# Performance work log

Hardware: AMD Instinct MI355X
Metric: run time of the kernel (lower is better)

## Reference

```python
import jax, jax.numpy as jnp
import numpy as np

GDEP = 3
ALPHA = 0.05


def setup_inputs() -> dict:
    key = jax.random.key(0)
    k1, k2, k3, k4 = jax.random.split(key, 4)
    x = jax.random.normal(k1, (8, 32, 512, 512), dtype=jnp.float32)
    adj = jax.random.uniform(k2, (512, 512), dtype=jnp.float32)
    W = jax.random.normal(k3, (32, 128), dtype=jnp.float32) * 0.02  # 1x1 conv weight [c_out, (gdep+1)*c_in]
    b = jax.random.normal(k4, (32,), dtype=jnp.float32) * 0.02
    return {"x": x, "adj": adj, "W": W, "b": b}


def reference(x, adj, W, b):
    # x: [n, c, v, l]; adj: [v, v]
    n_nodes = adj.shape[0]
    a = adj + jnp.eye(n_nodes, dtype=adj.dtype)
    a = a / a.sum(axis=1, keepdims=True)  # row-normalized adjacency
    h = x
    out = [h]
    for _ in range(GDEP):
        h = jnp.einsum('ncwl,vw->ncvl', h, a)       # diffuse over nodes
        h = ALPHA * x + (1.0 - ALPHA) * h           # alpha residual mix
        out.append(h)
    ho = jnp.concatenate(out, axis=1)               # [n, (gdep+1)*c, v, l]
    y = jnp.einsum('ncvl,oc->novl', ho, W) + b[None, :, None, None]  # 1x1 conv
    return y
```

## Files before the change

kernel.cpp:

```cpp
#include <hip/hip_runtime.h>
#include <cstdint>
#include <cstddef>

typedef unsigned short u16;
typedef unsigned int   u32;
typedef __attribute__((ext_vector_type(8))) short bf16x8;
typedef __attribute__((ext_vector_type(4))) float f32x4;

#define ALPHA 0.05f
#define OMA   0.95f

__device__ __forceinline__ u16 f2b(float f) {
  u32 u = __float_as_uint(f);
  u = (u + 0x7fffu + ((u >> 16) & 1u)) >> 16;
  return (u16)u;
}

__device__ __forceinline__ void gld16(const void* g, void* l) {
  __builtin_amdgcn_global_load_lds((const __attribute__((address_space(1))) u32*)g,
                                   (__attribute__((address_space(3))) u32*)l, 16, 0, 0);
}

__global__ __launch_bounds__(256) void k_norm(const float* __restrict__ adj,
                                              float* __restrict__ Af) {
  int v = blockIdx.x;
  int t = threadIdx.x;
  float a0 = adj[(size_t)v * 512 + t]       + (t == v ? 1.f : 0.f);
  float a1 = adj[(size_t)v * 512 + t + 256] + (t + 256 == v ? 1.f : 0.f);
  float s = a0 + a1;
  for (int off = 32; off; off >>= 1) s += __shfl_down(s, off);
  __shared__ float ws4[4];
  if ((t & 63) == 0) ws4[t >> 6] = s;
  __syncthreads();
  float inv = OMA / (ws4[0] + ws4[1] + ws4[2] + ws4[3]);
  Af[(size_t)v * 512 + t]       = a0 * inv;
  Af[(size_t)v * 512 + t + 256] = a1 * inv;
}

__global__ __launch_bounds__(256) void k_pow(const float* __restrict__ L,
                                             const float* __restrict__ R,
                                             float* __restrict__ Pf) {
  __shared__ float lrow[4][512];
  int r0 = blockIdx.x * 4;
  int t = threadIdx.x;
  for (int i = t; i < 4 * 512; i += 256)
    lrow[i >> 9][i & 511] = L[(size_t)(r0 + (i >> 9)) * 512 + (i & 511)];
  __syncthreads();
  float acc[4][2] = {};
  for (int k = 0; k < 512; ++k) {
    float rk0 = R[(size_t)k * 512 + t];
    float rk1 = R[(size_t)k * 512 + t + 256];
#pragma unroll
    for (int r = 0; r < 4; ++r) {
      float lv = lrow[r][k];
      acc[r][0] += lv * rk0;
      acc[r][1] += lv * rk1;
    }
  }
  for (int r = 0; r < 4; ++r) {
    Pf[(size_t)(r0 + r) * 512 + t]       = acc[r][0];
    Pf[(size_t)(r0 + r) * 512 + t + 256] = acc[r][1];
  }
}

__global__ __launch_bounds__(256) void k_pack(const float* __restrict__ A1,
                                              const float* __restrict__ A2,
                                              const float* __restrict__ A3,
                                              u16* __restrict__ G) {
  int v = blockIdx.x;
  int t = threadIdx.x;
#pragma unroll
  for (int h = 0; h < 2; ++h) {
    int w = t + h * 256;
    size_t i = (size_t)v * 512 + w;
    u32 lo = (u32)(w == v ? 0x3F80u : 0u) | ((u32)f2b(A1[i]) << 16);
    u32 hi = (u32)f2b(A2[i]) | ((u32)f2b(A3[i]) << 16);
    *(uint2*)(G + (size_t)v * 2048 + w * 4) = make_uint2(lo, hi);
  }
}

__global__ void k_u(const float* __restrict__ W, u16* __restrict__ U) {
  int R = threadIdx.x;
  int o = R >> 2, j = R & 3;
  for (int c = 0; c < 32; ++c) {
    float w0 = W[o * 128 + c];
    float w1 = W[o * 128 + 32 + c];
    float w2 = W[o * 128 + 64 + c];
    float w3 = W[o * 128 + 96 + c];
    float u;
    if (j == 0)      u = w0 + ALPHA * (w1 + w2 + w3);
    else if (j == 1) u = w1 + ALPHA * (w2 + w3);
    else if (j == 2) u = w2 + ALPHA * w3;
    else             u = w3;
    U[R * 32 + c] = f2b(u);
  }
}

__global__ __launch_bounds__(256) void k_mix(const float* __restrict__ x,
                                             const u16* __restrict__ Uw,
                                             u16* __restrict__ C,
                                             int n0) {
  __shared__ u16 slab[512 * 32];
  __shared__ u16 Ul[128 * 32];
  int t = threadIdx.x;
  int chunk = gridDim.x >> 3;
  int rb = blockIdx.x;
  int virt = (rb & 7) * chunk + (rb >> 3);
  int q  = virt & 511;
  int n  = n0 + (virt >> 9);
  int v0 = (q & 31) << 4;
  int l0 = (q >> 5) << 5;

  gld16(Uw + t * 8,        (char*)Ul + ((t >> 6) << 10));
  gld16(Uw + 2048 + t * 8, (char*)Ul + 4096 + ((t >> 6) << 10));

  int c = t & 31;
  int v = t >> 5;
#pragma unroll
  for (int h = 0; h < 2; ++h) {
    int vv = v + h * 8;
    const float* xp = x + (((size_t)(n * 32 + c) * 512 + v0 + vv) << 9) + l0;
#pragma unroll
    for (int f = 0; f < 8; ++f) {
      float4 d = *(const float4*)(xp + f * 4);
      int p = (f * 4) * 16 + vv;
      slab[(p + 0)  * 32 + c] = f2b(d.x);
      slab[(p + 16) * 32 + c] = f2b(d.y);
      slab[(p + 32) * 32 + c] = f2b(d.z);
      slab[(p + 48) * 32 + c] = f2b(d.w);
    }
  }
  __syncthreads();

  int lane = t & 63, wid = t >> 6;
  int l15 = lane & 15, g = lane >> 4;

  bf16x8 a[8], b[8];
#pragma unroll
  for (int mt = 0; mt < 8; ++mt)
    a[mt] = *(const bf16x8*)(Ul + (mt * 16 + l15) * 32 + g * 8);
#pragma unroll
  for (int i = 0; i < 8; ++i) {
    int p = (wid * 8 + i) * 16 + l15;
    b[i] = *(const bf16x8*)(slab + p * 32 + g * 8);
  }

  int nol_base = (n - n0) * 32;
  int w = v0 + l15;
#pragma unroll
  for (int mt = 0; mt < 8; ++mt) {
    int o = mt * 4 + g;
    u16* cbase = C + ((size_t)(nol_base + o) * 512 + l0) * 2048 + (size_t)w * 4;
#pragma unroll
    for (int i = 0; i < 8; ++i) {
      f32x4 z = {0.f, 0.f, 0.f, 0.f};
      f32x4 acc = __builtin_amdgcn_mfma_f32_16x16x32_bf16(a[mt], b[i], z, 0, 0, 0);
      int nt = wid * 8 + i;
      u32 lo = (u32)f2b(acc[0]) | ((u32)f2b(acc[1]) << 16);
      u32 hi = (u32)f2b(acc[2]) | ((u32)f2b(acc[3]) << 16);
      *(uint2*)(cbase + (size_t)nt * 2048) = make_uint2(lo, hi);
    }
  }
}

#define BAR   asm volatile("s_barrier" ::: "memory")
#define LGKM0 do { asm volatile("s_waitcnt lgkmcnt(0)" ::: "memory");          \
                   __builtin_amdgcn_sched_barrier(0); } while (0)
#define VM6   asm volatile("s_waitcnt vmcnt(6)" ::: "memory")
#define VM0   asm volatile("s_waitcnt vmcnt(0)" ::: "memory")

__global__ __launch_bounds__(512, 2) void k_gemm(const u16* __restrict__ G,
                                                 const u16* __restrict__ C,
                                                 const float* __restrict__ bias,
                                                 float* __restrict__ y,
                                                 int n0) {
  __shared__ u16 lds[65536];
  int t = threadIdx.x;
  int rb = blockIdx.x;
  int chunk = gridDim.x >> 3;
  int virt = (rb & 7) * chunk + (rb >> 3);
  int nn = n0 + (virt >> 7);
  int r7 = virt & 127;
  int o  = r7 >> 2;
  int vt = (r7 >> 1) & 1, lt = r7 & 1;
  int v0 = vt << 8, l0 = lt << 8;
  const u16* Cp = C + (size_t)((nn - n0) * 32 + o) * (512 * 2048);

  int lane = t & 63, wid = t >> 6;
  int l15 = lane & 15, g = lane >> 4;
  int wm = wid >> 2, wn = wid & 3;

  int rr = t >> 3;
  int sp = (t & 7) ^ (rr & 7);
  const u16* gA = G  + (size_t)(v0 + rr) * 2048 + sp * 8;
  const u16* gB = Cp + (size_t)(l0 + rr) * 2048 + sp * 8;
  char* ldsw = (char*)lds + (wid << 10);

#define STGA(b, T, h)                                                        \
  do {                                                                       \
    const u16* s_ = gA + (size_t)(h) * 262144 + (size_t)(T) * 64;            \
    gld16(s_,          ldsw + (b) * 32768 + (h) * 16384);                    \
    gld16(s_ + 131072, ldsw + (b) * 32768 + (h) * 16384 + 8192);             \
  } while (0)
#define STGB(b, T, h)                                                        \
  do {                                                                       \
    const u16* s_ = gB + (size_t)(h) * 262144 + (size_t)(T) * 64;            \
    gld16(s_,          ldsw + 65536 + (b) * 32768 + (h) * 16384);            \
    gld16(s_ + 131072, ldsw + 65536 + (b) * 32768 + (h) * 16384 + 8192);     \
  } while (0)

  int sx0 = (g ^ (l15 & 7)) << 4;
  int sx1 = ((4 | g) ^ (l15 & 7)) << 4;
  int aoff = (wm * 128 + l15) * 128;
  int boff = (wn * 64 + l15) * 128;
  const char* ldsc = (const char*)lds;

  bf16x8 af[8][2], bf[4][2];
#define RDALL(b)                                                             \
  do {                                                                       \
    _Pragma("unroll") for (int m = 0; m < 8; ++m) {                          \
      af[m][0] = *(const bf16x8*)(ldsc + (b) * 32768 + aoff + m * 2048 + sx0); \
      af[m][1] = *(const bf16x8*)(ldsc + (b) * 32768 + aoff + m * 2048 + sx1); \
    }                                                                        \
    _Pragma("unroll") for (int n = 0; n < 4; ++n) {                          \
      bf[n][0] = *(const bf16x8*)(ldsc + 65536 + (b) * 32768 + boff + n * 2048 + sx0); \
      bf[n][1] = *(const bf16x8*)(ldsc + 65536 + (b) * 32768 + boff + n * 2048 + sx1); \
    }                                                                        \
  } while (0)

  f32x4 acc[8][4];
#pragma unroll
  for (int i = 0; i < 8; ++i)
#pragma unroll
    for (int j = 0; j < 4; ++j) {
      f32x4 z = {0.f, 0.f, 0.f, 0.f};
      acc[i][j] = z;
    }

#define CLUSTER(mh, ks)                                                      \
  do {                                                                       \
    __builtin_amdgcn_s_setprio(1);                                           \
    _Pragma("unroll") for (int m = 0; m < 4; ++m)                            \
    _Pragma("unroll") for (int n = 0; n < 4; ++n)                            \
      acc[(mh) * 4 + m][n] = __builtin_amdgcn_mfma_f32_16x16x32_bf16(        \
          af[(mh) * 4 + m][ks], bf[n][ks], acc[(mh) * 4 + m][n], 0, 0, 0);   \
    __builtin_amdgcn_s_setprio(0);                                           \
  } while (0)

  STGA(0, 0, 0); STGA(0, 0, 1); STGB(0, 0, 0); STGB(0, 0, 1);
  STGA(1, 1, 0); STGA(1, 1, 1); STGB(1, 1, 0);
  VM6;
  BAR;

  for (int tt = 0; tt < 16; ++tt) {
    int t1 = 2 * tt + 1;
    int T2 = 2 * tt + 2;
    int T3 = 2 * tt + 3;
    bool more = (tt < 15);
    RDALL(0);
    STGB(1, t1, 1);
    BAR; LGKM0;
    CLUSTER(0, 0); BAR;
    if (more) STGA(0, T2, 0);
    BAR; CLUSTER(0, 1); BAR;
    if (more) STGA(0, T2, 1);
    BAR; CLUSTER(1, 0); BAR;
    if (more) {
      STGB(0, T2, 0);
      VM6;
    } else {
      VM0;
    }
    BAR; CLUSTER(1, 1); BAR;
    RDALL(1);
    if (more) STGB(0, T2, 1);
    BAR; LGKM0;
    CLUSTER(0, 0); BAR;
    if (more) STGA(1, T3, 0);
    BAR; CLUSTER(0, 1); BAR;
    if (more) STGA(1, T3, 1);
    BAR; CLUSTER(1, 0); BAR;
    if (more) {
      STGB(1, T3, 0);
      VM6;
    }
    BAR; CLUSTER(1, 1); BAR;
  }
#undef STGA
#undef STGB
#undef RDALL
#undef CLUSTER

  float bo = bias[o];
#pragma unroll
  for (int mm = 0; mm < 8; ++mm)
#pragma unroll
    for (int n = 0; n < 4; ++n)
#pragma unroll
      for (int q = 0; q < 4; ++q) {
        int vv = v0 + wm * 128 + mm * 16 + g * 4 + q;
        int ll = l0 + wn * 64 + n * 16 + l15;
        size_t idx = (((size_t)(nn * 32 + o) * 512 + vv) << 9) + ll;
        y[idx] = acc[mm][n][q] + bo;
      }
}

extern "C" void kernel_launch(void* const* d_in, const int* in_sizes, int n_in,
                              void* d_out, int out_size, void* d_ws, size_t ws_size,
                              hipStream_t stream) {
  (void)in_sizes; (void)n_in; (void)out_size;
  const float* x    = (const float*)d_in[0];
  const float* adj  = (const float*)d_in[1];
  const float* W    = (const float*)d_in[2];
  const float* bias = (const float*)d_in[3];
  float* y = (float*)d_out;
  char* ws = (char*)d_ws;

  u16*   G  = (u16*)(ws);
  float* Af = (float*)(ws + 2097152);
  float* A2 = (float*)(ws + 3145728);
  float* A3 = (float*)(ws + 4194304);
  u16*   U  = (u16*)(ws + 5242880);
  u16*   C  = (u16*)(ws + 5251072);
  const size_t fixed = 5251072;
  const size_t per_n = (size_t)32 * 512 * 2048 * 2;

  int grp = 0;
  const int cands[4] = {8, 4, 2, 1};
  for (int i = 0; i < 4; ++i)
    if (fixed + (size_t)cands[i] * per_n <= ws_size) { grp = cands[i]; break; }
  if (!grp) return;

  k_norm<<<dim3(512), dim3(256), 0, stream>>>(adj, Af);
  k_pow <<<dim3(128), dim3(256), 0, stream>>>(Af, Af, A2);
  k_pow <<<dim3(128), dim3(256), 0, stream>>>(A2, Af, A3);
  k_pack<<<dim3(512), dim3(256), 0, stream>>>(Af, A2, A3, G);
  k_u   <<<dim3(1),   dim3(128), 0, stream>>>(W, U);

  for (int n0 = 0; n0 < 8; n0 += grp) {
    k_mix <<<dim3(grp * 512), dim3(256), 0, stream>>>(x, U, C, n0);
    k_gemm<<<dim3(grp * 128), dim3(512), 0, stream>>>(G, C, bias, y, n0);
  }
}
```

Before: 495.0 us.

## Split LDS fragment reads by k-slice and reorder MFMA clusters to overlap reads

The single LDS read of all fragments per stage is split into two halves by k-slice. The first MFMA cluster now starts once only the k=0 fragments are issued, and the k=1 reads overlap with it. The cluster order changes to (0,0),(1,0),(0,1),(1,1), and the global-to-LDS staging is rescheduled so the vmcnt wait drops from 6 to 4. Sched barriers are added after the vmcnt waits. The risk is a hazard: CLUSTER(0,0) issues without an explicit lgkmcnt wait on the k=0 reads, so correctness depends on the compiler inserting the waits.

```diff
diff --git a/kernel.cpp b/kernel.cpp
--- a/kernel.cpp
+++ b/kernel.cpp
@@ -166,8 +166,10 @@
 #define BAR   asm volatile("s_barrier" ::: "memory")
 #define LGKM0 do { asm volatile("s_waitcnt lgkmcnt(0)" ::: "memory");          \
                    __builtin_amdgcn_sched_barrier(0); } while (0)
-#define VM6   asm volatile("s_waitcnt vmcnt(6)" ::: "memory")
-#define VM0   asm volatile("s_waitcnt vmcnt(0)" ::: "memory")
+#define VM4   do { asm volatile("s_waitcnt vmcnt(4)" ::: "memory");            \
+                   __builtin_amdgcn_sched_barrier(0); } while (0)
+#define VM0   do { asm volatile("s_waitcnt vmcnt(0)" ::: "memory");            \
+                   __builtin_amdgcn_sched_barrier(0); } while (0)
 
 __global__ __launch_bounds__(512, 2) void k_gemm(const u16* __restrict__ G,
                                                  const u16* __restrict__ C,
@@ -216,16 +218,19 @@
   const char* ldsc = (const char*)lds;
 
   bf16x8 af[8][2], bf[4][2];
-#define RDALL(b)                                                             \
-  do {                                                                       \
-    _Pragma("unroll") for (int m = 0; m < 8; ++m) {                          \
+#define RDK0(b)                                                              \
+  do {                                                                       \
+    _Pragma("unroll") for (int m = 0; m < 8; ++m)                            \
       af[m][0] = *(const bf16x8*)(ldsc + (b) * 32768 + aoff + m * 2048 + sx0); \
+    _Pragma("unroll") for (int n = 0; n < 4; ++n)                            \
+      bf[n][0] = *(const bf16x8*)(ldsc + 65536 + (b) * 32768 + boff + n * 2048 + sx0); \
+  } while (0)
+#define RDK1(b)                                                              \
+  do {                                                                       \
+    _Pragma("unroll") for (int m = 0; m < 8; ++m)                            \
       af[m][1] = *(const bf16x8*)(ldsc + (b) * 32768 + aoff + m * 2048 + sx1); \
-    }                                                                        \
-    _Pragma("unroll") for (int n = 0; n < 4; ++n) {                          \
-      bf[n][0] = *(const bf16x8*)(ldsc + 65536 + (b) * 32768 + boff + n * 2048 + sx0); \
+    _Pragma("unroll") for (int n = 0; n < 4; ++n)                            \
       bf[n][1] = *(const bf16x8*)(ldsc + 65536 + (b) * 32768 + boff + n * 2048 + sx1); \
-    }                                                                        \
   } while (0)
 
   f32x4 acc[8][4];
@@ -248,8 +253,8 @@
   } while (0)
 
   STGA(0, 0, 0); STGA(0, 0, 1); STGB(0, 0, 0); STGB(0, 0, 1);
-  STGA(1, 1, 0); STGA(1, 1, 1); STGB(1, 1, 0);
-  VM6;
+  STGA(1, 1, 0); STGA(1, 1, 1);
+  VM4;
   BAR;
 
   for (int tt = 0; tt < 16; ++tt) {
@@ -257,38 +262,39 @@
     int T2 = 2 * tt + 2;
     int T3 = 2 * tt + 3;
     bool more = (tt < 15);
-    RDALL(0);
+    RDK0(0);
+    STGB(1, t1, 0);
+    BAR; CLUSTER(0, 0); BAR;
+    RDK1(0);
     STGB(1, t1, 1);
-    BAR; LGKM0;
-    CLUSTER(0, 0); BAR;
+    BAR; CLUSTER(1, 0); LGKM0; BAR;
     if (more) STGA(0, T2, 0);
     BAR; CLUSTER(0, 1); BAR;
-    if (more) STGA(0, T2, 1);
-    BAR; CLUSTER(1, 0); BAR;
     if (more) {
-      STGB(0, T2, 0);
-      VM6;
+      STGA(0, T2, 1);
+      VM4;
     } else {
       VM0;
     }
     BAR; CLUSTER(1, 1); BAR;
-    RDALL(1);
+    RDK0(1);
+    if (more) STGB(0, T2, 0);
+    BAR; CLUSTER(0, 0); BAR;
+    RDK1(1);
     if (more) STGB(0, T2, 1);
-    BAR; LGKM0;
-    CLUSTER(0, 0); BAR;
+    BAR; CLUSTER(1, 0); LGKM0; BAR;
     if (more) STGA(1, T3, 0);
     BAR; CLUSTER(0, 1); BAR;
-    if (more) STGA(1, T3, 1);
-    BAR; CLUSTER(1, 0); BAR;
     if (more) {
-      STGB(1, T3, 0);
-      VM6;
+      STGA(1, T3, 1);
+      VM4;
     }
     BAR; CLUSTER(1, 1); BAR;
   }
 #undef STGA
 #undef STGB
-#undef RDALL
+#undef RDK0
+#undef RDK1
 #undef CLUSTER
 
   float bo = bias[o];
```

Result: no change. 493.2 us (-0.4%).

## Restructure GEMM main loop to interleave per-k-slice LDS reads with MFMA clusters

Applied to the files above, without the earlier changes.

Rewrites the double-buffered k_gemm main loop. The single bulk LDS read of a whole tile is split into per-k-slice reads of A rows 0-3, B and A rows 4-7, issued between MFMA clusters so operand fetch for the next slice overlaps compute on the current one. The explicit lgkmcnt waits and about half of the barriers are removed. In exchange, global prefetch now runs only one tile ahead, and it waits with vmcnt(0) rather than vmcnt(6), so more global-load latency may be exposed.

```diff
diff --git a/kernel.cpp b/kernel.cpp
--- a/kernel.cpp
+++ b/kernel.cpp
@@ -164,10 +164,8 @@
 }
 
 #define BAR   asm volatile("s_barrier" ::: "memory")
-#define LGKM0 do { asm volatile("s_waitcnt lgkmcnt(0)" ::: "memory");          \
+#define VM0   do { asm volatile("s_waitcnt vmcnt(0)" ::: "memory");            \
                    __builtin_amdgcn_sched_barrier(0); } while (0)
-#define VM6   asm volatile("s_waitcnt vmcnt(6)" ::: "memory")
-#define VM0   asm volatile("s_waitcnt vmcnt(0)" ::: "memory")
 
 __global__ __launch_bounds__(512, 2) void k_gemm(const u16* __restrict__ G,
                                                  const u16* __restrict__ C,
@@ -216,16 +214,23 @@
   const char* ldsc = (const char*)lds;
 
   bf16x8 af[8][2], bf[4][2];
-#define RDALL(b)                                                             \
-  do {                                                                       \
-    _Pragma("unroll") for (int m = 0; m < 8; ++m) {                          \
-      af[m][0] = *(const bf16x8*)(ldsc + (b) * 32768 + aoff + m * 2048 + sx0); \
-      af[m][1] = *(const bf16x8*)(ldsc + (b) * 32768 + aoff + m * 2048 + sx1); \
-    }                                                                        \
-    _Pragma("unroll") for (int n = 0; n < 4; ++n) {                          \
-      bf[n][0] = *(const bf16x8*)(ldsc + 65536 + (b) * 32768 + boff + n * 2048 + sx0); \
-      bf[n][1] = *(const bf16x8*)(ldsc + 65536 + (b) * 32768 + boff + n * 2048 + sx1); \
-    }                                                                        \
+#define RD_A03(b, ks)                                                        \
+  do {                                                                       \
+    int sx_ = (ks) ? sx1 : sx0;                                              \
+    _Pragma("unroll") for (int m = 0; m < 4; ++m)                            \
+      af[m][ks] = *(const bf16x8*)(ldsc + (b) * 32768 + aoff + m * 2048 + sx_); \
+  } while (0)
+#define RD_A47(b, ks)                                                        \
+  do {                                                                       \
+    int sx_ = (ks) ? sx1 : sx0;                                              \
+    _Pragma("unroll") for (int m = 4; m < 8; ++m)                            \
+      af[m][ks] = *(const bf16x8*)(ldsc + (b) * 32768 + aoff + m * 2048 + sx_); \
+  } while (0)
+#define RD_B(b, ks)                                                          \
+  do {                                                                       \
+    int sx_ = (ks) ? sx1 : sx0;                                              \
+    _Pragma("unroll") for (int n = 0; n < 4; ++n)                            \
+      bf[n][ks] = *(const bf16x8*)(ldsc + 65536 + (b) * 32768 + boff + n * 2048 + sx_); \
   } while (0)
 
   f32x4 acc[8][4];
@@ -248,47 +253,37 @@
   } while (0)
 
   STGA(0, 0, 0); STGA(0, 0, 1); STGB(0, 0, 0); STGB(0, 0, 1);
-  STGA(1, 1, 0); STGA(1, 1, 1); STGB(1, 1, 0);
-  VM6;
-  BAR;
+  VM0; BAR;
+  RD_A03(0, 0); RD_B(0, 0); RD_A47(0, 0);
 
   for (int tt = 0; tt < 16; ++tt) {
     int t1 = 2 * tt + 1;
     int T2 = 2 * tt + 2;
-    int T3 = 2 * tt + 3;
     bool more = (tt < 15);
-    RDALL(0);
-    STGB(1, t1, 1);
-    BAR; LGKM0;
+    RD_A03(0, 1); RD_B(0, 1); RD_A47(0, 1);
+    STGA(1, t1, 0); STGA(1, t1, 1);
     CLUSTER(0, 0); BAR;
-    if (more) STGA(0, T2, 0);
-    BAR; CLUSTER(0, 1); BAR;
-    if (more) STGA(0, T2, 1);
-    BAR; CLUSTER(1, 0); BAR;
-    if (more) {
-      STGB(0, T2, 0);
-      VM6;
-    } else {
-      VM0;
-    }
-    BAR; CLUSTER(1, 1); BAR;
-    RDALL(1);
-    if (more) STGB(0, T2, 1);
-    BAR; LGKM0;
+    STGB(1, t1, 0); STGB(1, t1, 1);
+    CLUSTER(1, 0); BAR;
+    VM0;
+    CLUSTER(0, 1); BAR;
+    RD_A03(1, 0); RD_B(1, 0); RD_A47(1, 0);
+    CLUSTER(1, 1); BAR;
+    RD_A03(1, 1); RD_B(1, 1); RD_A47(1, 1);
+    if (more) { STGA(0, T2, 0); STGA(0, T2, 1); }
     CLUSTER(0, 0); BAR;
-    if (more) STGA(1, T3, 0);
-    BAR; CLUSTER(0, 1); BAR;
-    if (more) STGA(1, T3, 1);
-    BAR; CLUSTER(1, 0); BAR;
-    if (more) {
-      STGB(1, T3, 0);
-      VM6;
-    }
-    BAR; CLUSTER(1, 1); BAR;
+    if (more) { STGB(0, T2, 0); STGB(0, T2, 1); }
+    CLUSTER(1, 0); BAR;
+    VM0;
+    CLUSTER(0, 1); BAR;
+    RD_A03(0, 0); RD_B(0, 0); RD_A47(0, 0);
+    CLUSTER(1, 1); BAR;
   }
 #undef STGA
 #undef STGB
-#undef RDALL
+#undef RD_A03
+#undef RD_A47
+#undef RD_B
 #undef CLUSTER
 
   float bo = bias[o];
```

Result: slower. 549.5 us (+11.0%).
